# Kernel tuning notes

Measured on AMD Instinct MI355X. Metric: run time of the kernel, lower is better.

Reference implementation:

```python
import jax, jax.numpy as jnp
import numpy as np

D_MODEL = 768
N_HEADS = 8
Q_RANK = 64
KV_RANK = 64
ROPE_DIM = 64
NOPE_DIM = D_MODEL // N_HEADS - ROPE_DIM  # 32
V_DIM = D_MODEL // N_HEADS               # 96
Q_HEAD_DIM = NOPE_DIM + ROPE_DIM         # 96
EPS = 1e-6
ROPE_BASE = 10000.0


def rms_norm(x, w, eps=EPS):
    v = jnp.mean(jnp.square(x.astype(jnp.float32)), axis=-1, keepdims=True)
    return (x.astype(jnp.float32) * jax.lax.rsqrt(v + eps)).astype(x.dtype) * w


def rope_cos_sin(seq_len, dim):
    inv_freq = 1.0 / (ROPE_BASE ** (jnp.arange(0, dim, 2, dtype=jnp.float32) / dim))
    freqs = jnp.outer(jnp.arange(seq_len, dtype=jnp.float32), inv_freq)
    emb = jnp.concatenate([freqs, freqs], axis=-1)  # [s, dim]
    return jnp.cos(emb), jnp.sin(emb)


def apply_rope(x, cos, sin, pos_ids):
    # x: [b,h,s,d]; DeepSeek-V2 de-interleaves pairs before rotate_half
    b, h, s, d = x.shape
    x = x.reshape(b, h, s, d // 2, 2).transpose(0, 1, 2, 4, 3).reshape(b, h, s, d)
    c = cos[pos_ids][:, None]  # [b,1,s,d]
    sn = sin[pos_ids][:, None]
    x1, x2 = jnp.split(x, 2, axis=-1)
    rot = jnp.concatenate([-x2, x1], axis=-1)
    return x * c + rot * sn


def setup_inputs() -> dict:
    key = jax.random.key(0)
    ks = jax.random.split(key, 8)
    s = 0.02
    return {
        "src": jax.random.normal(ks[0], (4, 2048, D_MODEL), jnp.float32),
        "wq_a": jax.random.normal(ks[1], (Q_RANK, D_MODEL), jnp.float32) * s,
        "q_a_ln_w": jnp.ones((Q_RANK,), jnp.float32),
        "wq_b": jax.random.normal(ks[2], (N_HEADS * Q_HEAD_DIM, Q_RANK), jnp.float32) * s,
        "wkv_a": jax.random.normal(ks[3], (KV_RANK + ROPE_DIM, D_MODEL), jnp.float32) * s,
        "kv_a_ln_w": jnp.ones((KV_RANK,), jnp.float32),
        "wkv_b": jax.random.normal(ks[4], (N_HEADS * (NOPE_DIM + V_DIM), KV_RANK), jnp.float32) * s,
        "wo": jax.random.normal(ks[5], (D_MODEL, N_HEADS * V_DIM), jnp.float32) * s,
        "norm_w": jnp.ones((D_MODEL,), jnp.float32),
    }


def reference(src, wq_a, q_a_ln_w, wq_b, wkv_a, kv_a_ln_w, wkv_b, wo, norm_w):
    b, s, _ = src.shape
    pos = jnp.broadcast_to(jnp.arange(s)[None], (b, s))
    cos, sin = rope_cos_sin(s, ROPE_DIM)

    # ---- compress_kv (torch.no_grad in original) ----
    ckv = src @ wkv_a.T                                  # [b,s,rank+rope]
    c_lat, k_pe = ckv[..., :KV_RANK], ckv[..., KV_RANK:]
    c_lat = rms_norm(c_lat, kv_a_ln_w)
    k_pe = apply_rope(k_pe[:, None], cos, sin, pos)[:, 0]  # [b,s,rope]
    c_lat = jax.lax.stop_gradient(c_lat)
    k_pe = jax.lax.stop_gradient(k_pe)

    # ---- query path ----
    q = rms_norm(src @ wq_a.T, q_a_ln_w) @ wq_b.T        # [b,s,h*96]
    q = q.reshape(b, s, N_HEADS, Q_HEAD_DIM).transpose(0, 2, 1, 3)
    q_nope, q_pe = q[..., :NOPE_DIM], q[..., NOPE_DIM:]
    q_pe = apply_rope(q_pe, cos, sin, pos)

    # ---- absorb kv_b_proj ----
    w = wkv_b.reshape(N_HEADS, NOPE_DIM + V_DIM, KV_RANK)
    q_absorb, out_absorb = w[:, :NOPE_DIM], w[:, NOPE_DIM:]   # [h,32,r], [h,96,r]
    q_lat = jnp.einsum('bhsd,hdr->bhsr', q_nope, q_absorb)    # [b,h,s,r]

    scale = Q_HEAD_DIM ** -0.5
    scores = (jnp.einsum('bhsr,btr->bhst', q_lat, c_lat)
              + jnp.einsum('bhsd,btd->bhst', q_pe, k_pe)) * scale
    attn = jax.nn.softmax(scores.astype(jnp.float32), axis=-1).astype(src.dtype)

    ctx = jnp.einsum('bhst,btr->bhsr', attn, c_lat)           # [b,h,s,r]
    ctx = jnp.einsum('bhsr,hvr->bhsv', ctx, out_absorb)       # [b,h,s,96]
    attn_out = ctx.transpose(0, 2, 1, 3).reshape(b, s, N_HEADS * V_DIM) @ wo.T

    # residual (dropout in eval = identity) + RMSNorm
    return rms_norm(src + attn_out, norm_w)
```

## Files before the change

kernel.cpp:

```cpp
#include <hip/hip_runtime.h>


#define DEV static __device__ __forceinline__
typedef unsigned short ushort_t;
typedef __attribute__((ext_vector_type(8))) short bf8_t;
typedef __attribute__((ext_vector_type(4))) float f4_t;

DEV float bf2f(unsigned int u) {
    union { float f; unsigned int i; } x; x.i = u << 16; return x.f;
}
DEV ushort_t f2bf(float f) {
    union { float f; unsigned int u; } x; x.f = f;
    unsigned int u = x.u;
    return (ushort_t)((u + 0x7fffu + ((u >> 16) & 1u)) >> 16);
}
DEV float ldin(const void* p, size_t i, int isbf) {
    return isbf ? bf2f(((const ushort_t*)p)[i]) : ((const float*)p)[i];
}
DEV float fexp2(float x) {
#if __has_builtin(__builtin_amdgcn_exp2f)
    return __builtin_amdgcn_exp2f(x);
#else
    return exp2f(x);
#endif
}
DEV int get_isbf(const void* nw) {
    return ((((const unsigned int*)nw)[0] & 0xffffu) != 0u) ? 1 : 0;
}

constexpr int   TOK   = 4 * 2048;
constexpr float EPSF  = 1e-6f;
constexpr float QSCALE = (float)(0.10206207261596575 * 1.4426950408889634);
constexpr float L2_10000_OVER_32 = 0.4152410118609203f;

constexpr size_t OFF_WOT   = 0;
constexpr size_t OFF_WKVAT = 589824;
constexpr size_t OFF_WQAT  = 688128;
constexpr size_t OFF_WQBT  = 737280;
constexpr size_t OFF_QAF   = 786432;
constexpr size_t OFF_OAT   = 802816;
constexpr size_t OFF_QLN   = 851968;
constexpr size_t OFF_KVLN  = 852032;
constexpr size_t OFF_NW    = 852096;
constexpr size_t OFF_FLAG  = 852864;
constexpr size_t OFF_CTXF  = 852880;
constexpr size_t OFF_SRCBF = 3998608;
constexpr size_t OFF_KBF   = 7144336;
constexpr size_t OFF_VTB   = 7668624;
constexpr size_t OFF_QBF   = 7930768;
constexpr size_t OFF_ROPE  = 12125072;

__global__ __launch_bounds__(256) void prep_k(
    const void* __restrict__ wq_a, const void* __restrict__ q_ln,
    const void* __restrict__ wq_b, const void* __restrict__ wkv_a,
    const void* __restrict__ kv_ln, const void* __restrict__ wkv_b,
    const void* __restrict__ wo, const void* __restrict__ nw,
    float* __restrict__ ws)
{
    const int isbf = get_isbf(nw);
    int i = blockIdx.x * 256 + threadIdx.x;
    int y = blockIdx.y;
    if (y == 0) {
        if (i < 768 * 768) {
            ushort_t* wob = (ushort_t*)(ws + OFF_WOT);
            wob[i] = isbf ? ((const ushort_t*)wo)[i] : f2bf(((const float*)wo)[i]);
        }
    } else if (y == 1) {
        if (i < 128 * 768) {
            ushort_t* d = (ushort_t*)(ws + OFF_WKVAT);
            d[i] = isbf ? ((const ushort_t*)wkv_a)[i] : f2bf(((const float*)wkv_a)[i]);
        }
    } else if (y == 2) {
        if (i < 64 * 768) {
            ushort_t* d = (ushort_t*)(ws + OFF_WQAT);
            d[i] = isbf ? ((const ushort_t*)wq_a)[i] : f2bf(((const float*)wq_a)[i]);
        }
    } else if (y == 3) {
        if (i < 768 * 64) {
            ushort_t* d = (ushort_t*)(ws + OFF_WQBT);
            d[i] = isbf ? ((const ushort_t*)wq_b)[i] : f2bf(((const float*)wq_b)[i]);
        }
    } else if (y == 4) {
        if (i < 8 * 64 * 32) {
            int h = i >> 11, rem = i & 2047, r = rem >> 5, d = rem & 31;
            ushort_t* dst = (ushort_t*)(ws + OFF_QAF);
            dst[i] = f2bf(ldin(wkv_b, (size_t)(h * 128 + d) * 64 + r, isbf) * QSCALE);
        }
    } else if (y == 5) {
        if (i < 8 * 64 * 96) {
            int h = i / 6144, rem = i - h * 6144;
            int r = rem / 96, v = rem - r * 96;
            ws[OFF_OAT + i] = ldin(wkv_b, (size_t)h * 8192 + 2048 + v * 64 + r, isbf);
        }
    } else if (y == 6) {
        if (i < 64)             ws[OFF_QLN + i]       = ldin(q_ln, i, isbf);
        else if (i < 128)       ws[OFF_KVLN + i - 64] = ldin(kv_ln, i - 64, isbf);
        else if (i < 128 + 768) ws[OFF_NW + i - 128]  = ldin(nw, i - 128, isbf);
    } else {
        if (i < 2048 * 32) {
            int pos = i >> 5, p = i & 31;
            float inv = exp2f(-(float)p * L2_10000_OVER_32);
            float ang = (float)pos * inv;
            float2* tab = (float2*)(ws + OFF_ROPE);
            tab[i] = make_float2(cosf(ang), sinf(ang));
        }
    }
}

__global__ __launch_bounds__(512) void k1_ckv(
    const void* __restrict__ src, const void* __restrict__ nw,
    const float* __restrict__ ws,
    ushort_t* __restrict__ Kbf, ushort_t* __restrict__ VTbf,
    ushort_t* __restrict__ srcbf)
{
    const ushort_t* wkvab = (const ushort_t*)(ws + OFF_WKVAT);
    const float* kvln  = ws + OFF_KVLN;
    const float2* tab  = (const float2*)(ws + OFF_ROPE);
    const int isbf = get_isbf(nw);
    __shared__ __align__(16) ushort_t sA[32 * 776];
    __shared__ float ckv[32][132];
    int j = threadIdx.x;
    int t0 = blockIdx.x * 32;
    int w = j >> 6, lane = j & 63;
    int tl = lane & 15, qd = lane >> 4;

    {
        for (int e = j; e < 32 * 96; e += 512) {
            int row = e / 96, c8 = e - row * 96;
            size_t off = (size_t)(t0 + row) * 768 + c8 * 8;
            if (isbf) {
                uint4 v = *(const uint4*)((const ushort_t*)src + off);
                *(uint4*)(sA + row * 776 + c8 * 8) = v;
            } else {
                const float4* p = (const float4*)((const float*)src + off);
                float4 f0 = p[0], f1 = p[1];
                ushort_t tmp[8] = {f2bf(f0.x), f2bf(f0.y), f2bf(f0.z), f2bf(f0.w),
                                   f2bf(f1.x), f2bf(f1.y), f2bf(f1.z), f2bf(f1.w)};
                uint4 v = *(const uint4*)tmp;
                *(uint4*)(sA + row * 776 + c8 * 8) = v;
                *(uint4*)(srcbf + off) = v;
            }
        }
    }
    __syncthreads();
    {
        f4_t acc[2];
        acc[0] = (f4_t){0.f, 0.f, 0.f, 0.f};
        acc[1] = (f4_t){0.f, 0.f, 0.f, 0.f};
        const ushort_t* bp = wkvab + (size_t)(w * 16 + tl) * 768 + qd * 8;
#pragma unroll 4
        for (int ks = 0; ks < 24; ++ks) {
            bf8_t b  = *(const bf8_t*)(bp + ks * 32);
            bf8_t a0 = *(const bf8_t*)(sA + tl * 776 + ks * 32 + qd * 8);
            bf8_t a1 = *(const bf8_t*)(sA + (16 + tl) * 776 + ks * 32 + qd * 8);
            acc[0] = __builtin_amdgcn_mfma_f32_16x16x32_bf16(a0, b, acc[0], 0, 0, 0);
            acc[1] = __builtin_amdgcn_mfma_f32_16x16x32_bf16(a1, b, acc[1], 0, 0, 0);
        }
#pragma unroll
        for (int mt = 0; mt < 2; ++mt)
#pragma unroll
            for (int r = 0; r < 4; ++r)
                ckv[mt * 16 + qd * 4 + r][w * 16 + tl] = acc[mt][r];
    }
    __syncthreads();

    if (j < 256) {
        int tt = j >> 3, l = j & 7;
        float ss = 0.f;
#pragma unroll
        for (int i = 0; i < 8; ++i) { float v = ckv[tt][l * 8 + i]; ss += v * v; }
        ss += __shfl_xor(ss, 1); ss += __shfl_xor(ss, 2); ss += __shfl_xor(ss, 4);
        float rs = rsqrtf(ss * (1.f / 64.f) + EPSF);
        size_t base = (size_t)(t0 + tt) * 128;
        ushort_t kb[8];
        float clw[8];
#pragma unroll
        for (int i = 0; i < 8; ++i) {
            int o2 = l * 8 + i;
            float cl = ckv[tt][o2] * rs;
            if (isbf) cl = bf2f(f2bf(cl));
            clw[i] = cl * kvln[o2];
            kb[i] = f2bf(clw[i]);
        }
        uint4 pack;
        pack.x = kb[0] | ((unsigned)kb[1] << 16); pack.y = kb[2] | ((unsigned)kb[3] << 16);
        pack.z = kb[4] | ((unsigned)kb[5] << 16); pack.w = kb[6] | ((unsigned)kb[7] << 16);
        *(uint4*)&Kbf[base + l * 8] = pack;
        int pos = (t0 + tt) & 2047;
        ushort_t r0[4], r1[4];
#pragma unroll
        for (int i = 0; i < 4; ++i) {
            int p = l * 4 + i;
            float2 cssn = tab[pos * 32 + p];
            float e = ckv[tt][64 + 2 * p], od = ckv[tt][64 + 2 * p + 1];
            r0[i] = f2bf(e * cssn.x - od * cssn.y);
            r1[i] = f2bf(od * cssn.x + e * cssn.y);
        }
        uint2 p0, p1;
        p0.x = r0[0] | ((unsigned)r0[1] << 16); p0.y = r0[2] | ((unsigned)r0[3] << 16);
        p1.x = r1[0] | ((unsigned)r1[1] << 16); p1.y = r1[2] | ((unsigned)r1[3] << 16);
        *(uint2*)&Kbf[base + 64 + l * 4] = p0;
        *(uint2*)&Kbf[base + 96 + l * 4] = p1;
#pragma unroll
        for (int i = 0; i < 8; ++i) ckv[tt][l * 8 + i] = clw[i];
    }
    __syncthreads();
    if (j < 256) {
        int t = j & 31, rb = (j >> 5) * 8;
        int bb = t0 >> 11, col = (t0 & 2047) + t;
#pragma unroll
        for (int i = 0; i < 8; ++i) {
            int r = rb + i;
            VTbf[((size_t)(bb * 64 + r)) * 2048 + col] = f2bf(ckv[t][r]);
        }
    }
}

__global__ __launch_bounds__(128) void k2_q(
    const void* __restrict__ src, const void* __restrict__ nw,
    const float* __restrict__ ws, ushort_t* __restrict__ Qbf)
{
    const int isbf = get_isbf(nw);
    const ushort_t* srcb = isbf ? (const ushort_t*)src : (const ushort_t*)(ws + OFF_SRCBF);
    const ushort_t* wqab = (const ushort_t*)(ws + OFF_WQAT);
    const ushort_t* wqbb = (const ushort_t*)(ws + OFF_WQBT);
    const ushort_t* qabs = (const ushort_t*)(ws + OFF_QAF);
    const float2*   tab  = (const float2*)(ws + OFF_ROPE);
    const float*    qln  = ws + OFF_QLN;

    __shared__ __align__(16) ushort_t LDS[2 * 3968];
    int j = threadIdx.x;
    int w = j >> 6, lane = j & 63;
    int tl = lane & 15, qd = lane >> 4;
    ushort_t* tmpn = LDS + w * 3968;
    ushort_t* qn   = tmpn + 1152;
    ushort_t* qf   = qn + 640;
    int tokw = blockIdx.x * 16;

    f4_t C1[4];
#pragma unroll
    for (int nt = 0; nt < 4; ++nt) C1[nt] = (f4_t){0.f, 0.f, 0.f, 0.f};
    {
        const ushort_t* ap = srcb + (size_t)(tokw + tl) * 768 + qd * 8;
#pragma unroll 4
        for (int ks = 0; ks < 24; ++ks) {
            bf8_t a = *(const bf8_t*)(ap + ks * 32);
#pragma unroll
            for (int nt = 0; nt < 4; ++nt) {
                bf8_t bfr = *(const bf8_t*)(wqab + (size_t)(nt * 16 + tl) * 768 + ks * 32 + qd * 8);
                C1[nt] = __builtin_amdgcn_mfma_f32_16x16x32_bf16(a, bfr, C1[nt], 0, 0, 0);
            }
        }
    }
    float rsv[4];
#pragma unroll
    for (int r = 0; r < 4; ++r) {
        float s = C1[0][r] * C1[0][r] + C1[1][r] * C1[1][r]
                + C1[2][r] * C1[2][r] + C1[3][r] * C1[3][r];
        s += __shfl_xor(s, 1); s += __shfl_xor(s, 2);
        s += __shfl_xor(s, 4); s += __shfl_xor(s, 8);
        rsv[r] = rsqrtf(s * (1.f / 64.f) + EPSF);
    }
    float qlnv[4];
#pragma unroll
    for (int nt = 0; nt < 4; ++nt) qlnv[nt] = qln[nt * 16 + tl];
#pragma unroll
    for (int nt = 0; nt < 4; ++nt)
#pragma unroll
        for (int r = 0; r < 4; ++r) {
            float v = C1[nt][r] * rsv[r];
            if (isbf) v = bf2f(f2bf(v));
            tmpn[(qd * 4 + r) * 72 + nt * 16 + tl] = f2bf(v * qlnv[nt]);
        }
    bf8_t A2[2];
#pragma unroll
    for (int ks = 0; ks < 2; ++ks) A2[ks] = *(const bf8_t*)(tmpn + tl * 72 + ks * 32 + qd * 8);

    float csv[4][4], snv[4][4];
#pragma unroll
    for (int nt2 = 0; nt2 < 4; ++nt2) {
        int p = (nt2 * 16 + tl) >> 1;
#pragma unroll
        for (int r = 0; r < 4; ++r) {
            int pos = (tokw + qd * 4 + r) & 2047;
            float2 t = tab[pos * 32 + p];
            csv[nt2][r] = t.x * QSCALE;
            snv[nt2][r] = t.y * QSCALE;
        }
    }
    const bool evn = !(tl & 1);
    int bb = tokw >> 11, pos0 = tokw & 2047;

    for (int h = w * 4; h < w * 4 + 4; ++h) {
        f4_t C2[6];
#pragma unroll
        for (int nt = 0; nt < 6; ++nt) C2[nt] = (f4_t){0.f, 0.f, 0.f, 0.f};
#pragma unroll
        for (int nt = 0; nt < 6; ++nt)
#pragma unroll
            for (int ks = 0; ks < 2; ++ks) {
                bf8_t bfr = *(const bf8_t*)(wqbb + (size_t)(h * 96 + nt * 16 + tl) * 64 + ks * 32 + qd * 8);
                C2[nt] = __builtin_amdgcn_mfma_f32_16x16x32_bf16(A2[ks], bfr, C2[nt], 0, 0, 0);
            }
#pragma unroll
        for (int nt = 0; nt < 2; ++nt)
#pragma unroll
            for (int r = 0; r < 4; ++r)
                qn[(qd * 4 + r) * 40 + nt * 16 + tl] = f2bf(C2[nt][r]);
        bf8_t an = *(const bf8_t*)(qn + tl * 40 + qd * 8);
        f4_t C3[4];
#pragma unroll
        for (int nt = 0; nt < 4; ++nt) C3[nt] = (f4_t){0.f, 0.f, 0.f, 0.f};
#pragma unroll
        for (int nt = 0; nt < 4; ++nt) {
            bf8_t bfr = *(const bf8_t*)(qabs + (size_t)h * 2048 + (nt * 16 + tl) * 32 + qd * 8);
            C3[nt] = __builtin_amdgcn_mfma_f32_16x16x32_bf16(an, bfr, C3[nt], 0, 0, 0);
        }
#pragma unroll
        for (int nt = 0; nt < 4; ++nt)
#pragma unroll
            for (int r = 0; r < 4; ++r)
                qf[(qd * 4 + r) * 136 + nt * 16 + tl] = f2bf(C3[nt][r]);
#pragma unroll
        for (int nt2 = 0; nt2 < 4; ++nt2) {
            int p = (nt2 * 16 + tl) >> 1;
            int outc = evn ? (64 + p) : (96 + p);
#pragma unroll
            for (int r = 0; r < 4; ++r) {
                float val = C2[nt2 + 2][r];
                float part = __shfl_xor(val, 1);
                float res = evn ? (val * csv[nt2][r] - part * snv[nt2][r])
                                : (val * csv[nt2][r] + part * snv[nt2][r]);
                qf[(qd * 4 + r) * 136 + outc] = f2bf(res);
            }
        }
        size_t qb = ((size_t)(bb * 8 + h) * 2048 + pos0) * 128;
#pragma unroll
        for (int i = 0; i < 4; ++i) {
            int idx = i * 64 + lane;
            int row = idx >> 4, c = idx & 15;
            uint4 v = *(const uint4*)(qf + row * 136 + c * 8);
            *(uint4*)(Qbf + qb + (size_t)row * 128 + c * 8) = v;
        }
    }
}

__global__ __launch_bounds__(256, 2) void k3_attn(
    const ushort_t* __restrict__ Qbf, const ushort_t* __restrict__ Kbf,
    const ushort_t* __restrict__ VTbf, const float* __restrict__ oaT,
    ushort_t* __restrict__ ctxb)
{
    __shared__ __align__(16) ushort_t LDS[22528];
    ushort_t* Kt = LDS;
    ushort_t* Vt = LDS + 8704;
    ushort_t* Pw = LDS + 13312;
    int j = threadIdx.x;
    int b = blockIdx.z, h = blockIdx.y, q0g = blockIdx.x * 128;
    int w = j >> 6, lane = j & 63;
    int tl = lane & 15, qd = lane >> 4;
    ushort_t* Pme = Pw + w * 2304;
    int qw = q0g + w * 32;

    bf8_t qfA[4], qfB[4];
    {
        const ushort_t* qp = Qbf + ((size_t)((b * 8 + h) * 2048) + qw + tl) * 128 + qd * 8;
#pragma unroll
        for (int ks = 0; ks < 4; ++ks) {
            qfA[ks] = *(const bf8_t*)(qp + ks * 32);
            qfB[ks] = *(const bf8_t*)(qp + 16 * 128 + ks * 32);
        }
    }
    f4_t OaccA[4], OaccB[4];
#pragma unroll
    for (int nt = 0; nt < 4; ++nt) {
        OaccA[nt] = (f4_t){0.f, 0.f, 0.f, 0.f};
        OaccB[nt] = (f4_t){0.f, 0.f, 0.f, 0.f};
    }
    float lA = 0.f, lB = 0.f;

    const size_t kbase = (size_t)b * 2048 * 128;
    const size_t vbase = (size_t)b * 64 * 2048;

    for (int it = 0; it < 32; ++it) {
        __syncthreads();
        {
            int r = j >> 2, c0 = (j & 3) * 32;
            const uint4* gp = (const uint4*)(Kbf + kbase + (size_t)(it * 64 + r) * 128 + c0);
            uint4 a0 = gp[0], a1 = gp[1], a2 = gp[2], a3 = gp[3];
            uint4* dp = (uint4*)(Kt + r * 136 + c0);
            dp[0] = a0; dp[1] = a1; dp[2] = a2; dp[3] = a3;
        }
        {
            int d = j >> 2, c0 = (j & 3) * 16;
            const uint4* gp = (const uint4*)(VTbf + vbase + (size_t)d * 2048 + it * 64 + c0);
            uint4 a0 = gp[0], a1 = gp[1];
            uint4* dp = (uint4*)(Vt + d * 72 + c0);
            dp[0] = a0; dp[1] = a1;
        }
        __syncthreads();
        f4_t SA[4], SB[4];
        __builtin_amdgcn_s_setprio(1);
#pragma unroll
        for (int nt = 0; nt < 4; ++nt) {
            f4_t cA = (f4_t){0.f, 0.f, 0.f, 0.f};
            f4_t cB = (f4_t){0.f, 0.f, 0.f, 0.f};
#pragma unroll
            for (int ks = 0; ks < 4; ++ks) {
                bf8_t kf = *(const bf8_t*)(Kt + (nt * 16 + tl) * 136 + ks * 32 + qd * 8);
                cA = __builtin_amdgcn_mfma_f32_16x16x32_bf16(kf, qfA[ks], cA, 0, 0, 0);
                cB = __builtin_amdgcn_mfma_f32_16x16x32_bf16(kf, qfB[ks], cB, 0, 0, 0);
            }
            SA[nt] = cA; SB[nt] = cB;
        }
        __builtin_amdgcn_s_setprio(0);
        float rsA = 0.f, rsB = 0.f;
#pragma unroll
        for (int nt = 0; nt < 4; ++nt)
#pragma unroll
            for (int r = 0; r < 4; ++r) {
                float pA = fexp2(SA[nt][r]); SA[nt][r] = pA; rsA += pA;
                float pB = fexp2(SB[nt][r]); SB[nt][r] = pB; rsB += pB;
            }
        rsA += __shfl_xor(rsA, 16); rsA += __shfl_xor(rsA, 32);
        rsB += __shfl_xor(rsB, 16); rsB += __shfl_xor(rsB, 32);
        lA += rsA; lB += rsB;
#pragma unroll
        for (int nt = 0; nt < 4; ++nt) {
            uint2 pkA, pkB;
            pkA.x = f2bf(SA[nt][0]) | ((unsigned)f2bf(SA[nt][1]) << 16);
            pkA.y = f2bf(SA[nt][2]) | ((unsigned)f2bf(SA[nt][3]) << 16);
            pkB.x = f2bf(SB[nt][0]) | ((unsigned)f2bf(SB[nt][1]) << 16);
            pkB.y = f2bf(SB[nt][2]) | ((unsigned)f2bf(SB[nt][3]) << 16);
            *(uint2*)(Pme + tl * 72 + nt * 16 + qd * 4) = pkA;
            *(uint2*)(Pme + (16 + tl) * 72 + nt * 16 + qd * 4) = pkB;
        }
        bf8_t pfA[2], pfB[2];
#pragma unroll
        for (int ks = 0; ks < 2; ++ks) {
            pfA[ks] = *(const bf8_t*)(Pme + tl * 72 + ks * 32 + qd * 8);
            pfB[ks] = *(const bf8_t*)(Pme + (16 + tl) * 72 + ks * 32 + qd * 8);
        }
        __builtin_amdgcn_s_setprio(1);
#pragma unroll
        for (int nt = 0; nt < 4; ++nt)
#pragma unroll
            for (int ks = 0; ks < 2; ++ks) {
                bf8_t vf = *(const bf8_t*)(Vt + (nt * 16 + tl) * 72 + ks * 32 + qd * 8);
                OaccA[nt] = __builtin_amdgcn_mfma_f32_16x16x32_bf16(pfA[ks], vf, OaccA[nt], 0, 0, 0);
                OaccB[nt] = __builtin_amdgcn_mfma_f32_16x16x32_bf16(pfB[ks], vf, OaccB[nt], 0, 0, 0);
            }
        __builtin_amdgcn_s_setprio(0);
    }
    {
        float linvA[4], linvB[4];
#pragma unroll
        for (int r = 0; r < 4; ++r) {
            float lqA = __shfl(lA, (lane & 48) + qd * 4 + r);
            float lqB = __shfl(lB, (lane & 48) + qd * 4 + r);
            linvA[r] = 1.f / lqA; linvB[r] = 1.f / lqB;
        }
#pragma unroll
        for (int nt = 0; nt < 4; ++nt)
#pragma unroll
            for (int r = 0; r < 4; ++r) {
                Pme[(qd * 4 + r) * 72 + nt * 16 + tl] = f2bf(OaccA[nt][r] * linvA[r]);
                Pme[(16 + qd * 4 + r) * 72 + nt * 16 + tl] = f2bf(OaccB[nt][r] * linvB[r]);
            }
    }
    __syncthreads();
    ushort_t* OA = LDS;
    for (int e = j; e < 96 * 64; e += 256) {
        int v = e >> 6, r = e & 63;
        OA[v * 72 + r] = f2bf(oaT[h * 6144 + r * 96 + v]);
    }
    __syncthreads();
    {
        bf8_t ofA[2], ofB[2];
#pragma unroll
        for (int ks = 0; ks < 2; ++ks) {
            ofA[ks] = *(const bf8_t*)(Pme + tl * 72 + ks * 32 + qd * 8);
            ofB[ks] = *(const bf8_t*)(Pme + (16 + tl) * 72 + ks * 32 + qd * 8);
        }
        __builtin_amdgcn_s_setprio(1);
#pragma unroll
        for (int nt = 0; nt < 6; ++nt) {
            f4_t cA = (f4_t){0.f, 0.f, 0.f, 0.f};
            f4_t cB = (f4_t){0.f, 0.f, 0.f, 0.f};
#pragma unroll
            for (int ks = 0; ks < 2; ++ks) {
                bf8_t af = *(const bf8_t*)(OA + (nt * 16 + tl) * 72 + ks * 32 + qd * 8);
                cA = __builtin_amdgcn_mfma_f32_16x16x32_bf16(ofA[ks], af, cA, 0, 0, 0);
                cB = __builtin_amdgcn_mfma_f32_16x16x32_bf16(ofB[ks], af, cB, 0, 0, 0);
            }
#pragma unroll
            for (int r = 0; r < 4; ++r) {
                size_t tokA = (size_t)(b * 2048 + qw + qd * 4 + r);
                size_t tokB = tokA + 16;
                ctxb[tokA * 768 + h * 96 + nt * 16 + tl] = f2bf(cA[r]);
                ctxb[tokB * 768 + h * 96 + nt * 16 + tl] = f2bf(cB[r]);
            }
        }
        __builtin_amdgcn_s_setprio(0);
    }
}

__global__ __launch_bounds__(256, 1) void k5_out(
    const void* __restrict__ src, const void* __restrict__ nw_in,
    const float* __restrict__ ws,
    const ushort_t* __restrict__ ctxb, void* __restrict__ out)
{
    const ushort_t* woB = (const ushort_t*)(ws + OFF_WOT);
    const float* nw = ws + OFF_NW;
    const int isbf = get_isbf(nw_in);
    __shared__ __align__(16) ushort_t ylds[32 * 776];
    int j = threadIdx.x;
    int t0 = blockIdx.x * 32;
    int w = j >> 6, lane = j & 63;
    int tl = lane & 15, qd = lane >> 4;
    int n0 = w * 192;

    {
        for (int e = j; e < 32 * 96; e += 256) {
            int row = e / 96, c16 = e - row * 96;
            uint4 v = *(const uint4*)(ctxb + (size_t)(t0 + row) * 768 + c16 * 8);
            *(uint4*)(ylds + row * 776 + c16 * 8) = v;
        }
    }
    __syncthreads();

    f4_t acc[2][12];
#pragma unroll
    for (int mt = 0; mt < 2; ++mt)
#pragma unroll
        for (int nt = 0; nt < 12; ++nt) acc[mt][nt] = (f4_t){0.f, 0.f, 0.f, 0.f};

#pragma unroll 2
    for (int ks = 0; ks < 24; ++ks) {
        bf8_t a0 = *(const bf8_t*)(ylds + tl * 776 + ks * 32 + qd * 8);
        bf8_t a1 = *(const bf8_t*)(ylds + (16 + tl) * 776 + ks * 32 + qd * 8);
#pragma unroll
        for (int nt = 0; nt < 12; ++nt) {
            bf8_t bfr = *(const bf8_t*)(woB + (size_t)(n0 + nt * 16 + tl) * 768 + ks * 32 + qd * 8);
            acc[0][nt] = __builtin_amdgcn_mfma_f32_16x16x32_bf16(a0, bfr, acc[0][nt], 0, 0, 0);
            acc[1][nt] = __builtin_amdgcn_mfma_f32_16x16x32_bf16(a1, bfr, acc[1][nt], 0, 0, 0);
        }
    }
    __syncthreads();

    {
#pragma unroll
        for (int mt = 0; mt < 2; ++mt)
#pragma unroll
            for (int nt = 0; nt < 12; ++nt)
#pragma unroll
                for (int r = 0; r < 4; ++r) {
                    int trow = mt * 16 + qd * 4 + r;
                    int col = n0 + nt * 16 + tl;
                    float yv = acc[mt][nt][r] + ldin(src, (size_t)(t0 + trow) * 768 + col, isbf);
                    ylds[trow * 776 + col] = f2bf(yv);
                }
    }
    __syncthreads();
    {
        int tt = j >> 3, sub = j & 7;
        const ushort_t* yp = ylds + tt * 776 + sub * 96;
        float ss = 0.f;
#pragma unroll
        for (int c = 0; c < 96; ++c) { float v = bf2f(yp[c]); ss += v * v; }
        ss += __shfl_xor(ss, 1); ss += __shfl_xor(ss, 2); ss += __shfl_xor(ss, 4);
        float rs = rsqrtf(ss * (1.f / 768.f) + EPSF);
        size_t base = (size_t)(t0 + tt) * 768 + sub * 96;
        if (isbf) {
            ushort_t* op = (ushort_t*)out + base;
#pragma unroll
            for (int c8 = 0; c8 < 12; ++c8) {
                ushort_t tmp[8];
#pragma unroll
                for (int c = 0; c < 8; ++c) {
                    float yv = bf2f(yp[c8 * 8 + c]);
                    float hv = bf2f(f2bf(yv * rs));
                    tmp[c] = f2bf(hv * nw[sub * 96 + c8 * 8 + c]);
                }
                *(uint4*)(op + c8 * 8) = *(const uint4*)tmp;
            }
        } else {
            float* op = (float*)out + base;
#pragma unroll
            for (int c = 0; c < 96; ++c) {
                float yv = bf2f(yp[c]);
                op[c] = yv * rs * nw[sub * 96 + c];
            }
        }
    }
}

extern "C" void kernel_launch(void* const* d_in, const int* in_sizes, int n_in,
                              void* d_out, int out_size, void* d_ws, size_t ws_size,
                              hipStream_t stream)
{
    const void* src   = d_in[0];
    const void* wq_a  = d_in[1];
    const void* q_ln  = d_in[2];
    const void* wq_b  = d_in[3];
    const void* wkv_a = d_in[4];
    const void* kv_ln = d_in[5];
    const void* wkv_b = d_in[6];
    const void* wo    = d_in[7];
    const void* nw    = d_in[8];
    float* ws = (float*)d_ws;
    ushort_t* Kbf   = (ushort_t*)(ws + OFF_KBF);
    ushort_t* VTbf  = (ushort_t*)(ws + OFF_VTB);
    ushort_t* Qbf   = (ushort_t*)(ws + OFF_QBF);
    ushort_t* ctxb  = (ushort_t*)(ws + OFF_CTXF);
    ushort_t* srcbf = (ushort_t*)(ws + OFF_SRCBF);

    prep_k<<<dim3(2304, 8), dim3(256), 0, stream>>>(wq_a, q_ln, wq_b, wkv_a, kv_ln, wkv_b, wo, nw, ws);
    k1_ckv<<<dim3(TOK / 32), dim3(512), 0, stream>>>(src, nw, ws, Kbf, VTbf, srcbf);
    k2_q<<<dim3(TOK / 16), dim3(128), 0, stream>>>(src, nw, ws, Qbf);
    k3_attn<<<dim3(16, 8, 4), dim3(256), 0, stream>>>(Qbf, Kbf, VTbf, ws + OFF_OAT, ctxb);
    k5_out<<<dim3(TOK / 32), dim3(256), 0, stream>>>(src, nw, ws, ctxb, d_out);
}
```

Before: 299.4 us.

## Split output projection and final RMSNorm into separate kernels for more parallelism

```diff
diff --git a/kernel.cpp b/kernel.cpp
--- a/kernel.cpp
+++ b/kernel.cpp
@@ -504,92 +504,107 @@
     }
 }
 
-__global__ __launch_bounds__(256, 1) void k5_out(
-    const void* __restrict__ src, const void* __restrict__ nw_in,
+__global__ __launch_bounds__(512, 2) void k5a_gemm(
+    const void* __restrict__ src, const void* __restrict__ nw,
     const float* __restrict__ ws,
-    const ushort_t* __restrict__ ctxb, void* __restrict__ out)
+    const ushort_t* __restrict__ ctxb, ushort_t* __restrict__ ybf)
 {
     const ushort_t* woB = (const ushort_t*)(ws + OFF_WOT);
+    const int isbf = get_isbf(nw);
+    __shared__ __align__(16) ushort_t sA[32 * 776];
+    int j = threadIdx.x;
+    int bx = blockIdx.x;
+    int t0 = (bx >> 1) * 32;
+    int colh = (bx & 1) * 384;
+    int w = j >> 6, lane = j & 63;
+    int tl = lane & 15, qd = lane >> 4;
+    int mt = w & 1;
+    int n0 = colh + (w >> 1) * 96;
+
+    {
+        for (int e = j; e < 32 * 96; e += 512) {
+            int row = e / 96, c8 = e - row * 96;
+            uint4 v = *(const uint4*)(ctxb + (size_t)(t0 + row) * 768 + c8 * 8);
+            *(uint4*)(sA + row * 776 + c8 * 8) = v;
+        }
+    }
+    __syncthreads();
+
+    f4_t acc[6];
+#pragma unroll
+    for (int nt = 0; nt < 6; ++nt) acc[nt] = (f4_t){0.f, 0.f, 0.f, 0.f};
+    const ushort_t* ap = sA + (mt * 16 + tl) * 776 + qd * 8;
+#pragma unroll 4
+    for (int ks = 0; ks < 24; ++ks) {
+        bf8_t a = *(const bf8_t*)(ap + ks * 32);
+#pragma unroll
+        for (int nt = 0; nt < 6; ++nt) {
+            bf8_t bfr = *(const bf8_t*)(woB + (size_t)(n0 + nt * 16 + tl) * 768 + ks * 32 + qd * 8);
+            acc[nt] = __builtin_amdgcn_mfma_f32_16x16x32_bf16(a, bfr, acc[nt], 0, 0, 0);
+        }
+    }
+#pragma unroll
+    for (int nt = 0; nt < 6; ++nt)
+#pragma unroll
+        for (int r = 0; r < 4; ++r) {
+            int row = t0 + mt * 16 + qd * 4 + r;
+            int col = n0 + nt * 16 + tl;
+            float yv = acc[nt][r] + ldin(src, (size_t)row * 768 + col, isbf);
+            ybf[(size_t)row * 768 + col] = f2bf(yv);
+        }
+}
+
+__global__ __launch_bounds__(256) void k5b_norm(
+    const void* __restrict__ nw_in, const float* __restrict__ ws,
+    const ushort_t* __restrict__ ybf, void* __restrict__ out)
+{
     const float* nw = ws + OFF_NW;
     const int isbf = get_isbf(nw_in);
-    __shared__ __align__(16) ushort_t ylds[32 * 776];
     int j = threadIdx.x;
-    int t0 = blockIdx.x * 32;
-    int w = j >> 6, lane = j & 63;
-    int tl = lane & 15, qd = lane >> 4;
-    int n0 = w * 192;
-
-    {
-        for (int e = j; e < 32 * 96; e += 256) {
-            int row = e / 96, c16 = e - row * 96;
-            uint4 v = *(const uint4*)(ctxb + (size_t)(t0 + row) * 768 + c16 * 8);
-            *(uint4*)(ylds + row * 776 + c16 * 8) = v;
-        }
-    }
-    __syncthreads();
-
-    f4_t acc[2][12];
-#pragma unroll
-    for (int mt = 0; mt < 2; ++mt)
-#pragma unroll
-        for (int nt = 0; nt < 12; ++nt) acc[mt][nt] = (f4_t){0.f, 0.f, 0.f, 0.f};
-
-#pragma unroll 2
-    for (int ks = 0; ks < 24; ++ks) {
-        bf8_t a0 = *(const bf8_t*)(ylds + tl * 776 + ks * 32 + qd * 8);
-        bf8_t a1 = *(const bf8_t*)(ylds + (16 + tl) * 776 + ks * 32 + qd * 8);
-#pragma unroll
-        for (int nt = 0; nt < 12; ++nt) {
-            bf8_t bfr = *(const bf8_t*)(woB + (size_t)(n0 + nt * 16 + tl) * 768 + ks * 32 + qd * 8);
-            acc[0][nt] = __builtin_amdgcn_mfma_f32_16x16x32_bf16(a0, bfr, acc[0][nt], 0, 0, 0);
-            acc[1][nt] = __builtin_amdgcn_mfma_f32_16x16x32_bf16(a1, bfr, acc[1][nt], 0, 0, 0);
-        }
-    }
-    __syncthreads();
-
-    {
-#pragma unroll
-        for (int mt = 0; mt < 2; ++mt)
-#pragma unroll
-            for (int nt = 0; nt < 12; ++nt)
-#pragma unroll
-                for (int r = 0; r < 4; ++r) {
-                    int trow = mt * 16 + qd * 4 + r;
-                    int col = n0 + nt * 16 + tl;
-                    float yv = acc[mt][nt][r] + ldin(src, (size_t)(t0 + trow) * 768 + col, isbf);
-                    ylds[trow * 776 + col] = f2bf(yv);
-                }
-    }
-    __syncthreads();
-    {
-        int tt = j >> 3, sub = j & 7;
-        const ushort_t* yp = ylds + tt * 776 + sub * 96;
-        float ss = 0.f;
-#pragma unroll
-        for (int c = 0; c < 96; ++c) { float v = bf2f(yp[c]); ss += v * v; }
-        ss += __shfl_xor(ss, 1); ss += __shfl_xor(ss, 2); ss += __shfl_xor(ss, 4);
-        float rs = rsqrtf(ss * (1.f / 768.f) + EPSF);
-        size_t base = (size_t)(t0 + tt) * 768 + sub * 96;
-        if (isbf) {
-            ushort_t* op = (ushort_t*)out + base;
-#pragma unroll
-            for (int c8 = 0; c8 < 12; ++c8) {
-                ushort_t tmp[8];
-#pragma unroll
-                for (int c = 0; c < 8; ++c) {
-                    float yv = bf2f(yp[c8 * 8 + c]);
-                    float hv = bf2f(f2bf(yv * rs));
-                    tmp[c] = f2bf(hv * nw[sub * 96 + c8 * 8 + c]);
-                }
-                *(uint4*)(op + c8 * 8) = *(const uint4*)tmp;
-            }
-        } else {
-            float* op = (float*)out + base;
-#pragma unroll
-            for (int c = 0; c < 96; ++c) {
-                float yv = bf2f(yp[c]);
-                op[c] = yv * rs * nw[sub * 96 + c];
-            }
+    int tt = j >> 4, s = j & 15;
+    size_t row = (size_t)blockIdx.x * 16 + tt;
+    const ushort_t* yp = ybf + row * 768 + s * 48;
+
+    float val[48];
+    float ss = 0.f;
+#pragma unroll
+    for (int c8 = 0; c8 < 6; ++c8) {
+        union { uint4 u; ushort_t h[8]; } uu;
+        uu.u = ((const uint4*)yp)[c8];
+#pragma unroll
+        for (int c = 0; c < 8; ++c) {
+            float v = bf2f(uu.h[c]);
+            val[c8 * 8 + c] = v;
+            ss += v * v;
+        }
+    }
+    ss += __shfl_xor(ss, 1); ss += __shfl_xor(ss, 2);
+    ss += __shfl_xor(ss, 4); ss += __shfl_xor(ss, 8);
+    float rs = rsqrtf(ss * (1.f / 768.f) + EPSF);
+    const float* nwp = nw + s * 48;
+    size_t base = row * 768 + s * 48;
+    if (isbf) {
+        ushort_t* op = (ushort_t*)out + base;
+#pragma unroll
+        for (int c8 = 0; c8 < 6; ++c8) {
+            union { uint4 u; ushort_t h[8]; } uu;
+#pragma unroll
+            for (int c = 0; c < 8; ++c) {
+                float hv = bf2f(f2bf(val[c8 * 8 + c] * rs));
+                uu.h[c] = f2bf(hv * nwp[c8 * 8 + c]);
+            }
+            ((uint4*)op)[c8] = uu.u;
+        }
+    } else {
+        float* op = (float*)out + base;
+#pragma unroll
+        for (int c4 = 0; c4 < 12; ++c4) {
+            float4 f;
+            f.x = val[c4 * 4 + 0] * rs * nwp[c4 * 4 + 0];
+            f.y = val[c4 * 4 + 1] * rs * nwp[c4 * 4 + 1];
+            f.z = val[c4 * 4 + 2] * rs * nwp[c4 * 4 + 2];
+            f.w = val[c4 * 4 + 3] * rs * nwp[c4 * 4 + 3];
+            ((float4*)op)[c4] = f;
         }
     }
 }
@@ -613,10 +628,12 @@
     ushort_t* Qbf   = (ushort_t*)(ws + OFF_QBF);
     ushort_t* ctxb  = (ushort_t*)(ws + OFF_CTXF);
     ushort_t* srcbf = (ushort_t*)(ws + OFF_SRCBF);
+    ushort_t* ybf   = Qbf;
 
     prep_k<<<dim3(2304, 8), dim3(256), 0, stream>>>(wq_a, q_ln, wq_b, wkv_a, kv_ln, wkv_b, wo, nw, ws);
     k1_ckv<<<dim3(TOK / 32), dim3(512), 0, stream>>>(src, nw, ws, Kbf, VTbf, srcbf);
     k2_q<<<dim3(TOK / 16), dim3(128), 0, stream>>>(src, nw, ws, Qbf);
     k3_attn<<<dim3(16, 8, 4), dim3(256), 0, stream>>>(Qbf, Kbf, VTbf, ws + OFF_OAT, ctxb);
-    k5_out<<<dim3(TOK / 32), dim3(256), 0, stream>>>(src, nw, ws, ctxb, d_out);
-}
+    k5a_gemm<<<dim3(TOK / 32 * 2), dim3(512), 0, stream>>>(src, nw, ws, ctxb, ybf);
+    k5b_norm<<<dim3(TOK / 16), dim3(256), 0, stream>>>(nw, ws, ybf, d_out);
+}
```

After: 305.9 us. +2.2%, slower.
